# Optimization experiments

Measured on AMD Instinct MI355X. Metric: run time of the kernel, lower is better.

Reference implementation:

```python
import jax, jax.numpy as jnp
import numpy as np
import math

B, S, D, H = 1, 2048, 2048, 16
DH, DHID, DKER = 128, 256, 128  # dim_head, dim_hid, dim_ker


def _uniform(k, shape, a):
    return jax.random.uniform(k, shape, jnp.float32, -a, a)


def setup_inputs() -> dict:
    key = jax.random.key(0)
    ks = jax.random.split(key, 14)
    a1 = math.sqrt(6.0 / (DH + DHID))
    a2 = math.sqrt(6.0 / (DKER + DHID))
    a3 = math.sqrt(6.0 / (2 * DKER))
    return {
        "x_t": jax.random.normal(ks[0], (B, S, D), jnp.float32),
        "q": jax.random.normal(ks[1], (B, S, D), jnp.float32),
        "k": jax.random.normal(ks[2], (B, S, D), jnp.float32),
        "v": jax.random.normal(ks[3], (B, S, D), jnp.float32),
        "lr_attn_mask": jax.random.bernoulli(ks[4], 0.5, (B, H, S, S)),
        "sparse_norms_lse": jax.random.normal(ks[5], (B, H, S, 1), jnp.float32),
        "sparse_attn_weights": jax.random.normal(ks[6], (B, H, S, S), jnp.float32),
        "lambda_constant": 0,
        "kernel_q_mat1": _uniform(ks[7], (H, DH, DHID), a1),
        "kernel_k_mat1": _uniform(ks[8], (H, DH, DHID), a1),
        "kernel_q_mat2": _uniform(ks[9], (H, DHID, DKER), a2),
        "kernel_k_mat2": _uniform(ks[10], (H, DHID, DKER), a2),
        "interaction_k": _uniform(ks[11], (H, DKER, DKER), a3),
        "scalingD": jnp.full((1, H, 1, DKER), 1e-4, jnp.float32),
        "scalingD2": jnp.full((1, H, 1, DKER), 1e-4, jnp.float32),
    }


def _gelu(x):
    return jax.nn.gelu(x, approximate=False)  # matches torch F.gelu default


def reference(x_t, q, k, v, lr_attn_mask, sparse_norms_lse, sparse_attn_weights,
              lambda_constant, kernel_q_mat1, kernel_k_mat1, kernel_q_mat2,
              kernel_k_mat2, interaction_k, scalingD, scalingD2):
    Bq, Sq, Dq = q.shape
    dh = Dq // H
    # [B,S,D] -> [B,H,S,dh]
    qh = q.reshape(Bq, Sq, H, dh).transpose(0, 2, 1, 3)
    kh = k.reshape(Bq, Sq, H, dh).transpose(0, 2, 1, 3)
    vh = v.reshape(Bq, Sq, H, dh).transpose(0, 2, 1, 3)

    # per-head two-layer feature maps (dropout is identity at eval)
    qf = _gelu(jnp.einsum('bhsd,hde->bhse', qh, kernel_q_mat1))
    qf = _gelu(jnp.einsum('bhse,hef->bhsf', qf, kernel_q_mat2))
    kf = _gelu(jnp.einsum('bhsd,hde->bhse', kh, kernel_k_mat1))
    kf = jnp.abs(scalingD) * _gelu(jnp.einsum('bhse,hef->bhsf', kf, kernel_k_mat2))
    kf = kf + jnp.einsum('bhse,hef->bhsf', kf, interaction_k) * scalingD2

    # masked non-negative kernel scores [B,H,S,S]
    scores = jnp.einsum('bhse,bhte->bhst', jnp.abs(qf), jnp.abs(kf))
    m = lr_attn_mask.astype(scores.dtype)
    scores = m * scores

    lr_norms_lse = jnp.log(scores.sum(axis=-1, keepdims=True) + 1e-6)
    norm_factor_lse = jnp.logaddexp(lr_norms_lse, sparse_norms_lse)

    logits = jnp.log(scores + 1e-6) * m + (1.0 - m) * sparse_attn_weights
    attn = jnp.exp(logits - norm_factor_lse)

    out = jnp.einsum('bhst,bhtd->bhsd', attn, vh)
    return out.transpose(0, 2, 1, 3).reshape(Bq, Sq, Dq)
```

## Files before the change

kernel.cpp:

```cpp
#include <hip/hip_runtime.h>
#include <hip/hip_bf16.h>
#include <math.h>

#define H_    16
#define S_    2048
#define D_    2048
#define DH_   128
#define DHID_ 256
#define DKER_ 128

typedef __attribute__((ext_vector_type(8))) short short8v;
typedef __attribute__((ext_vector_type(4))) float float4v;
typedef __attribute__((ext_vector_type(4))) int int4v;

static __device__ __forceinline__ short f2bf(float x){
  union { float f; unsigned u; } v; v.f = x;
  unsigned r = v.u + 0x7fffu + ((v.u >> 16) & 1u);
  return (short)(r >> 16);
}
static __device__ __forceinline__ float gelu_f(float x){
  return 0.5f * x * (1.0f + erff(x * 0.70710678118654752440f));
}
static __device__ __forceinline__ float4v mfma16(short8v a, short8v b, float4v c){
  return __builtin_amdgcn_mfma_f32_16x16x32_bf16(a, b, c, 0, 0, 0);
}
static __device__ __forceinline__ unsigned cvtpk(float lo, float hi){
  unsigned d;
  asm("v_cvt_pk_bf16_f32 %0, %1, %2" : "=v"(d) : "v"(lo), "v"(hi));
  return d;
}
static __device__ __forceinline__ void glds16(const void* g, void* l){
  __builtin_amdgcn_global_load_lds(
      (const __attribute__((address_space(1))) void*)g,
      (__attribute__((address_space(3))) void*)l, 16, 0, 0);
}

__global__ void detect_mask_kernel(const unsigned int* mw, int* flag){
  int t = threadIdx.x;
  int bin = 1, f32ok = 1, odd0 = 1;
  for (int i = t; i < 1024; i += 256){
    unsigned w = mw[i];
    if (w > 1u) bin = 0;
    if (w != 0u && w != 0x3F800000u) f32ok = 0;
    if ((i & 1) && w != 0u) odd0 = 0;
  }
  __shared__ int sb, sf, so;
  if (t == 0){ sb = 1; sf = 1; so = 1; }
  __syncthreads();
  if (!bin)  atomicAnd(&sb, 0);
  if (!f32ok) atomicAnd(&sf, 0);
  if (!odd0) atomicAnd(&so, 0);
  __syncthreads();
  if (t == 0) *flag = sb ? (so ? 3 : 0) : (sf ? 2 : 1);
}

__global__ __launch_bounds__(256) void prep_kernel(
    const void* __restrict__ mask, const int* __restrict__ flagp,
    unsigned* __restrict__ MP,
    const float* __restrict__ w1q, short* __restrict__ W1qT,
    const float* __restrict__ w1k, short* __restrict__ W1kT,
    const float* __restrict__ w2q, short* __restrict__ W2qT,
    const float* __restrict__ w2k, short* __restrict__ W2kT,
    const float* __restrict__ ik,  short* __restrict__ IKT,
    const float* __restrict__ v,   short* __restrict__ V2){
  __shared__ float tile[32][33];
  int b = blockIdx.x;
  int tid = threadIdx.x;

  if (b < 8192){
    int flag = *flagp;
    size_t w = (size_t)b * 256 + tid;
    size_t base = w * 32;
    unsigned bits = 0;
    if (flag == 0){
      const int4v* m = (const int4v*)((const int*)mask + base);
      #pragma unroll
      for (int c = 0; c < 8; ++c){
        int4v x = m[c];
        bits |= (x[0] != 0 ? 1u : 0u) << (c*4+0);
        bits |= (x[1] != 0 ? 1u : 0u) << (c*4+1);
        bits |= (x[2] != 0 ? 1u : 0u) << (c*4+2);
        bits |= (x[3] != 0 ? 1u : 0u) << (c*4+3);
      }
    } else if (flag == 1){
      const int4v* m = (const int4v*)((const unsigned char*)mask + base);
      #pragma unroll
      for (int c = 0; c < 2; ++c){
        int4v x = m[c];
        #pragma unroll
        for (int e = 0; e < 4; ++e){
          unsigned u = (unsigned)x[e];
          #pragma unroll
          for (int bb = 0; bb < 4; ++bb)
            bits |= (((u >> (8*bb)) & 0xffu) != 0 ? 1u : 0u) << (c*16 + e*4 + bb);
        }
      }
    } else if (flag == 2){
      const float4v* m = (const float4v*)((const float*)mask + base);
      #pragma unroll
      for (int c = 0; c < 8; ++c){
        float4v x = m[c];
        bits |= (x[0] != 0.0f ? 1u : 0u) << (c*4+0);
        bits |= (x[1] != 0.0f ? 1u : 0u) << (c*4+1);
        bits |= (x[2] != 0.0f ? 1u : 0u) << (c*4+2);
        bits |= (x[3] != 0.0f ? 1u : 0u) << (c*4+3);
      }
    } else {
      const int4v* m = (const int4v*)((const int*)mask + 2*base);
      #pragma unroll
      for (int c = 0; c < 16; ++c){
        int4v x = m[c];
        bits |= (x[0] != 0 ? 1u : 0u) << (c*2+0);
        bits |= (x[2] != 0 ? 1u : 0u) << (c*2+1);
      }
    }
    MP[w] = bits;
    return;
  }
  b -= 8192;
  if (b < 2048){
    int h = b >> 7, bx = b & 127;
    int d = tid & 127, oct = tid >> 7;
    int t8 = bx * 2 + oct;
    const float* src = v + (size_t)(t8 * 8) * D_ + h * DH_ + d;
    short8v o;
    #pragma unroll
    for (int j = 0; j < 8; ++j) o[j] = f2bf(src[(size_t)j * D_]);
    *(short8v*)(V2 + (((size_t)h * (S_/8) + t8) * DH_ + d) * 8) = o;
    return;
  }
  b -= 2048;
  const float* src; short* dst; int R, C, bx, by, h;
  if (b < 512){        src = w1q; dst = W1qT; R = DH_;  C = DHID_;
                       bx = b & 7; by = (b >> 3) & 3; h = b >> 5; }
  else if (b < 1024){  b -= 512;  src = w1k; dst = W1kT; R = DH_;  C = DHID_;
                       bx = b & 7; by = (b >> 3) & 3; h = b >> 5; }
  else if (b < 1536){  b -= 1024; src = w2q; dst = W2qT; R = DHID_; C = DKER_;
                       bx = b & 3; by = (b >> 2) & 7; h = b >> 5; }
  else if (b < 2048){  b -= 1536; src = w2k; dst = W2kT; R = DHID_; C = DKER_;
                       bx = b & 3; by = (b >> 2) & 7; h = b >> 5; }
  else {               b -= 2048; src = ik;  dst = IKT;  R = DKER_; C = DKER_;
                       bx = b & 3; by = (b >> 2) & 3; h = b >> 4; }
  int tx = tid & 31, ty = tid >> 5;
  int c0 = bx * 32, r0 = by * 32;
  const float* s = src + (size_t)h * R * C;
  short* d = dst + (size_t)h * R * C;
  #pragma unroll
  for (int i = 0; i < 32; i += 8)
    tile[ty + i][tx] = s[(size_t)(r0 + ty + i) * C + (c0 + tx)];
  __syncthreads();
  #pragma unroll
  for (int i = 0; i < 32; i += 8)
    d[(size_t)(c0 + ty + i) * R + (r0 + tx)] = f2bf(tile[tx][ty + i]);
}

__global__ __launch_bounds__(256) void feat_kernel(
    const float* __restrict__ q, const float* __restrict__ k,
    const short* __restrict__ W1qT, const short* __restrict__ W2qT,
    const short* __restrict__ W1kT, const short* __restrict__ W2kT,
    const short* __restrict__ IKT, const float* __restrict__ sD,
    const float* __restrict__ sD2,
    short* __restrict__ QF, short* __restrict__ KF){
  __shared__ __align__(16) short yls[4][16][264];
  int z = blockIdx.y;
  bool isq = z < 16;
  int h = z & 15;
  const float* X = isq ? q : k;
  const short* W1T = isq ? W1qT : W1kT;
  const short* W2T = isq ? W2qT : W2kT;
  int lane = threadIdx.x & 63, warp = threadIdx.x >> 6;
  int s0 = (blockIdx.x * 4 + warp) * 16;
  int col = lane & 15, rg = lane >> 4;
  short8v a[4];
  {
    const float* xr = X + (size_t)(s0 + col) * D_ + h * DH_;
    #pragma unroll
    for (int kb = 0; kb < 4; ++kb){
      int k0 = kb * 32 + rg * 8;
      float4v x0 = *(const float4v*)(xr + k0);
      float4v x1 = *(const float4v*)(xr + k0 + 4);
      short8v t;
      t[0]=f2bf(x0[0]); t[1]=f2bf(x0[1]); t[2]=f2bf(x0[2]); t[3]=f2bf(x0[3]);
      t[4]=f2bf(x1[0]); t[5]=f2bf(x1[1]); t[6]=f2bf(x1[2]); t[7]=f2bf(x1[3]);
      a[kb] = t;
    }
  }
  const short* wbase = W1T + (size_t)h * DHID_ * DH_;
  #pragma unroll
  for (int j = 0; j < 16; ++j){
    int n = j * 16;
    float4v c = {0.f, 0.f, 0.f, 0.f};
    const short* wr = wbase + (size_t)(n + col) * DH_ + rg * 8;
    #pragma unroll
    for (int kb = 0; kb < 4; ++kb)
      c = mfma16(a[kb], *(const short8v*)(wr + kb * 32), c);
    #pragma unroll
    for (int r = 0; r < 4; ++r)
      yls[warp][rg * 4 + r][n + col] = f2bf(gelu_f(c[r]));
  }
  short8v a2[8];
  #pragma unroll
  for (int kb = 0; kb < 8; ++kb)
    a2[kb] = *(const short8v*)(&yls[warp][col][kb * 32 + rg * 8]);
  const short* wb2 = W2T + (size_t)h * DKER_ * DHID_;

  if (isq){
    short* qb = QF + ((size_t)h * S_ + s0) * DKER_;
    #pragma unroll
    for (int j = 0; j < 8; ++j){
      int n = j * 16;
      float4v c = {0.f, 0.f, 0.f, 0.f};
      const short* wr = wb2 + (size_t)(n + col) * DHID_ + rg * 8;
      #pragma unroll
      for (int kb = 0; kb < 8; ++kb)
        c = mfma16(a2[kb], *(const short8v*)(wr + kb * 32), c);
      #pragma unroll
      for (int r = 0; r < 4; ++r)
        qb[(size_t)(rg * 4 + r) * DKER_ + n + col] = f2bf(fabsf(gelu_f(c[r])));
    }
    return;
  }
  float kf0[8][4];
  #pragma unroll
  for (int j = 0; j < 8; ++j){
    int n = j * 16;
    float4v c = {0.f, 0.f, 0.f, 0.f};
    const short* wr = wb2 + (size_t)(n + col) * DHID_ + rg * 8;
    #pragma unroll
    for (int kb = 0; kb < 8; ++kb)
      c = mfma16(a2[kb], *(const short8v*)(wr + kb * 32), c);
    float sc = fabsf(sD[h * DKER_ + n + col]);
    #pragma unroll
    for (int r = 0; r < 4; ++r) kf0[j][r] = sc * gelu_f(c[r]);
  }
  #pragma unroll
  for (int j = 0; j < 8; ++j)
    #pragma unroll
    for (int r = 0; r < 4; ++r)
      yls[warp][rg * 4 + r][j * 16 + col] = f2bf(kf0[j][r]);
  short8v pa[4];
  #pragma unroll
  for (int kb = 0; kb < 4; ++kb)
    pa[kb] = *(const short8v*)(&yls[warp][col][kb * 32 + rg * 8]);
  const short* ib = IKT + (size_t)h * DKER_ * DKER_;
  short* ko = KF + ((size_t)h * S_ + s0) * DKER_;
  #pragma unroll
  for (int j = 0; j < 8; ++j){
    int n = j * 16;
    float4v c = {0.f, 0.f, 0.f, 0.f};
    const short* ir = ib + (size_t)(n + col) * DKER_ + rg * 8;
    #pragma unroll
    for (int kb = 0; kb < 4; ++kb)
      c = mfma16(pa[kb], *(const short8v*)(ir + kb * 32), c);
    float s2 = sD2[h * DKER_ + n + col];
    #pragma unroll
    for (int r = 0; r < 4; ++r)
      ko[(size_t)(rg * 4 + r) * DKER_ + n + col] = f2bf(fabsf(kf0[j][r] + c[r] * s2));
  }
}

__global__ __launch_bounds__(512, 4) void main_attn_kernel(
    const short* __restrict__ QF, const short* __restrict__ KF,
    const short* __restrict__ V2, const unsigned* __restrict__ MP,
    const float* __restrict__ SW, const float* __restrict__ LSE,
    float* __restrict__ OUT){
  __shared__ __align__(16) char smem[65536];
  int tid = threadIdx.x;
  int lane = tid & 63, warp = tid >> 6;
  int hf = warp >> 2, w4 = warp & 3;
  int flat = blockIdx.y * 32 + blockIdx.x;
  int nf = (flat & 7) * 64 + (flat >> 3);
  int sblk = nf & 31, h = nf >> 5;
  int tbase = hf * (S_ / 2);
  int s0 = (sblk * 4 + w4) * 16;
  int col = lane & 15, rg = lane >> 4;

  short* kbuf = (short*)(smem + hf * 32768);
  short* vbuf = (short*)(smem + hf * 32768 + 16384);

  short8v qa[4];
  const short* qr = QF + ((size_t)h * S_ + s0 + col) * DKER_ + rg * 8;
  #pragma unroll
  for (int kb = 0; kb < 4; ++kb) qa[kb] = *(const short8v*)(qr + kb * 32);

  float4v acc[8];
  #pragma unroll
  for (int j = 0; j < 8; ++j) acc[j] = (float4v){0.f, 0.f, 0.f, 0.f};
  float rs = 0.f;

  const char* kf_base = (const char*)(KF + ((size_t)h * S_ + tbase) * DKER_);
  const char* v2_base = (const char*)(V2 + ((size_t)h * (S_/8) + (tbase >> 3)) * DH_ * 8);
  int c0 = w4 * 64 + lane, c1 = c0 + 256;
  int kg0 = (c0 * 16) ^ (((c0 >> 4) & 7) << 4);
  int kg1 = (c1 * 16) ^ (((c1 >> 4) & 7) << 4);
  int vg0 = c0 * 16, vg1 = c1 * 16;
  int lds_lo = w4 * 512, lds_hi = 2048 + w4 * 512;

  const float* swrow = SW + ((size_t)h * S_ + s0 + col) * S_ + tbase + rg * 4;
  const unsigned* mpr = MP + ((size_t)h * S_ + s0 + col) * (S_ / 32) + (tbase >> 5);

  {
    glds16(kf_base + kg0, &kbuf[lds_lo]);
    glds16(kf_base + kg1, &kbuf[lds_hi]);
    glds16(v2_base + vg0, &vbuf[lds_lo]);
    glds16(v2_base + vg1, &vbuf[lds_hi]);
  }
  __syncthreads();

  int swz = (col & 7) << 4;
  int rowb0 = col * 256 + rg * 16;
  int ga = col + ((2 * (rg & 1)) << 4);
  int gb = ga + 16;
  bool hi = (rg >= 2);
  const int NITER = (S_ / 2) / 32;

  for (int ti = 0; ti < NITER; ++ti){
    int cur = ti & 1;
    if (ti + 1 < NITER){
      const char* kt = kf_base + (size_t)(ti + 1) * 8192;
      const char* vt = v2_base + (size_t)(ti + 1) * 8192;
      glds16(kt + kg0, &kbuf[(cur ^ 1) * 4096 + lds_lo]);
      glds16(kt + kg1, &kbuf[(cur ^ 1) * 4096 + lds_hi]);
      glds16(vt + vg0, &vbuf[(cur ^ 1) * 4096 + lds_lo]);
      glds16(vt + vg1, &vbuf[(cur ^ 1) * 4096 + lds_hi]);
    }
    const char* kbp = (const char*)kbuf + cur * 8192;
    const char* vbp = (const char*)vbuf + cur * 8192;

    float4v q0 = {0.f,0.f,0.f,0.f}, q1 = {0.f,0.f,0.f,0.f};
    #pragma unroll
    for (int kk = 0; kk < 4; ++kk){
      short8v a0 = *(const short8v*)(kbp + ((rowb0 + kk * 64) ^ swz));
      short8v a1 = *(const short8v*)(kbp + ((rowb0 + 4096 + kk * 64) ^ swz));
      q0 = mfma16(a0, qa[kk], q0);
      q1 = mfma16(a1, qa[kk], q1);
    }

    const float* swp = swrow + ti * 32;
    float4v sv0 = *(const float4v*)swp;
    float4v sv1 = *(const float4v*)(swp + 16);
    unsigned mw = mpr[ti];
    float p0[4], p1[4];
    #pragma unroll
    for (int r = 0; r < 4; ++r){
      bool m0 = (mw >> (rg * 4 + r)) & 1u;
      bool m1 = (mw >> (16 + rg * 4 + r)) & 1u;
      p0[r] = m0 ? (q0[r] + 1e-6f) : __expf(sv0[r]);
      p1[r] = m1 ? (q1[r] + 1e-6f) : __expf(sv1[r]);
      if (m0) rs += q0[r];
      if (m1) rs += q1[r];
    }
    unsigned k00 = cvtpk(p0[0], p0[1]), k01 = cvtpk(p0[2], p0[3]);
    unsigned k10 = cvtpk(p1[0], p1[1]), k11 = cvtpk(p1[2], p1[3]);
    unsigned a0 = __shfl((int)k00, ga), b0 = __shfl((int)k10, ga);
    unsigned a1 = __shfl((int)k01, ga), b1 = __shfl((int)k11, ga);
    unsigned a2 = __shfl((int)k00, gb), b2 = __shfl((int)k10, gb);
    unsigned a3 = __shfl((int)k01, gb), b3 = __shfl((int)k11, gb);
    union { unsigned u[4]; short8v v8; } pw;
    pw.u[0] = hi ? b0 : a0; pw.u[1] = hi ? b1 : a1;
    pw.u[2] = hi ? b2 : a2; pw.u[3] = hi ? b3 : a3;
    short8v pa = pw.v8;

    #pragma unroll
    for (int j = 0; j < 8; ++j){
      short8v vf = *(const short8v*)(vbp + rg * 2048 + (j * 16 + col) * 16);
      acc[j] = mfma16(pa, vf, acc[j]);
    }
    __syncthreads();
  }

  rs += __shfl_xor(rs, 16);
  rs += __shfl_xor(rs, 32);

  __syncthreads();
  float* cb = (float*)smem;
  float* rb = (float*)(smem + 32768);
  if (hf == 1){
    float* cw = cb + (size_t)w4 * 16 * 128;
    #pragma unroll
    for (int j = 0; j < 8; ++j)
      #pragma unroll
      for (int r = 0; r < 4; ++r)
        cw[(size_t)(rg * 4 + r) * 128 + j * 16 + col] = acc[j][r];
    if (lane < 16) rb[w4 * 16 + lane] = rs;
  }
  __syncthreads();
  if (hf == 0){
    float* cw = cb + (size_t)w4 * 16 * 128;
    #pragma unroll
    for (int j = 0; j < 8; ++j)
      #pragma unroll
      for (int r = 0; r < 4; ++r)
        acc[j][r] += cw[(size_t)(rg * 4 + r) * 128 + j * 16 + col];
    rs += rb[w4 * 16 + col];

    float a = logf(rs + 1e-6f);
    float b = LSE[h * S_ + s0 + col];
    float mx = fmaxf(a, b);
    float sc_col = expf(-(mx + log1pf(expf(-fabsf(a - b)))));
    float scale[4];
    #pragma unroll
    for (int r = 0; r < 4; ++r) scale[r] = __shfl(sc_col, rg * 4 + r);
    float* ob = OUT + (size_t)s0 * D_ + h * DH_;
    #pragma unroll
    for (int j = 0; j < 8; ++j)
      #pragma unroll
      for (int r = 0; r < 4; ++r)
        ob[(size_t)(rg * 4 + r) * D_ + j * 16 + col] = acc[j][r] * scale[r];
  }
}

extern "C" void kernel_launch(void* const* d_in, const int* in_sizes, int n_in,
                              void* d_out, int out_size, void* d_ws, size_t ws_size,
                              hipStream_t stream){
  (void)in_sizes; (void)n_in; (void)out_size; (void)ws_size;
  const float* q   = (const float*)d_in[1];
  const float* k   = (const float*)d_in[2];
  const float* v   = (const float*)d_in[3];
  const void*  msk = d_in[4];
  const float* lse = (const float*)d_in[5];
  const float* sw  = (const float*)d_in[6];
  const float* w1q = (const float*)d_in[8];
  const float* w1k = (const float*)d_in[9];
  const float* w2q = (const float*)d_in[10];
  const float* w2k = (const float*)d_in[11];
  const float* ik  = (const float*)d_in[12];
  const float* sD  = (const float*)d_in[13];
  const float* sD2 = (const float*)d_in[14];
  float* out = (float*)d_out;

  char* ws = (char*)d_ws;
  size_t o = 0;
  int*   flag = (int*)(ws);            o += 256;
  short* W1qT = (short*)(ws + o);      o += (size_t)H_ * DHID_ * DH_ * 2;
  short* W1kT = (short*)(ws + o);      o += (size_t)H_ * DHID_ * DH_ * 2;
  short* W2qT = (short*)(ws + o);      o += (size_t)H_ * DKER_ * DHID_ * 2;
  short* W2kT = (short*)(ws + o);      o += (size_t)H_ * DKER_ * DHID_ * 2;
  short* IKT  = (short*)(ws + o);      o += (size_t)H_ * DKER_ * DKER_ * 2;
  short* V2   = (short*)(ws + o);      o += (size_t)S_ * D_ * 2;
  short* QFb  = (short*)(ws + o);      o += (size_t)H_ * S_ * DKER_ * 2;
  short* KFb  = (short*)(ws + o);      o += (size_t)H_ * S_ * DKER_ * 2;
  unsigned* MP = (unsigned*)(ws + o);  o += (size_t)H_ * S_ * (S_/32) * 4;

  detect_mask_kernel<<<1, 256, 0, stream>>>((const unsigned int*)msk, flag);
  prep_kernel<<<12544, 256, 0, stream>>>(msk, flag, MP,
      w1q, W1qT, w1k, W1kT, w2q, W2qT, w2k, W2kT, ik, IKT, v, V2);

  feat_kernel<<<dim3(S_/64, 32), 256, 0, stream>>>(q, k,
      W1qT, W2qT, W1kT, W2kT, IKT, sD, sD2, QFb, KFb);

  main_attn_kernel<<<dim3(32, 16), 512, 0, stream>>>(
      QFb, KFb, V2, MP, sw, lse, out);
}
```

Baseline: 248.4 us.

## Fold mask detection into prep, prefetch sparse weights, permute V to drop shuffles

Drops the separate single-block mask-format detection kernel; every mask-packing block of prep_kernel now recomputes the format flag from the first 1024 words, saving a launch and the serialized dependency. The V bf16 packing is permuted so each lane's P fragment already matches the MFMA B-operand ordering, which removes the eight cross-lane shuffles and selects per iteration in the attention loop. The sparse-weight and mask-bit loads for the next tile are issued one iteration ahead to hide global latency. This adds redundant detection reads in 8192 blocks and extra registers for the prefetched values.

```diff
diff --git a/kernel.cpp b/kernel.cpp
--- a/kernel.cpp
+++ b/kernel.cpp
@@ -35,27 +35,8 @@
       (__attribute__((address_space(3))) void*)l, 16, 0, 0);
 }
 
-__global__ void detect_mask_kernel(const unsigned int* mw, int* flag){
-  int t = threadIdx.x;
-  int bin = 1, f32ok = 1, odd0 = 1;
-  for (int i = t; i < 1024; i += 256){
-    unsigned w = mw[i];
-    if (w > 1u) bin = 0;
-    if (w != 0u && w != 0x3F800000u) f32ok = 0;
-    if ((i & 1) && w != 0u) odd0 = 0;
-  }
-  __shared__ int sb, sf, so;
-  if (t == 0){ sb = 1; sf = 1; so = 1; }
-  __syncthreads();
-  if (!bin)  atomicAnd(&sb, 0);
-  if (!f32ok) atomicAnd(&sf, 0);
-  if (!odd0) atomicAnd(&so, 0);
-  __syncthreads();
-  if (t == 0) *flag = sb ? (so ? 3 : 0) : (sf ? 2 : 1);
-}
-
 __global__ __launch_bounds__(256) void prep_kernel(
-    const void* __restrict__ mask, const int* __restrict__ flagp,
+    const void* __restrict__ mask,
     unsigned* __restrict__ MP,
     const float* __restrict__ w1q, short* __restrict__ W1qT,
     const float* __restrict__ w1k, short* __restrict__ W1kT,
@@ -64,11 +45,30 @@
     const float* __restrict__ ik,  short* __restrict__ IKT,
     const float* __restrict__ v,   short* __restrict__ V2){
   __shared__ float tile[32][33];
+  __shared__ int sb, sf, so, sflag;
   int b = blockIdx.x;
   int tid = threadIdx.x;
 
   if (b < 8192){
-    int flag = *flagp;
+    {
+      const unsigned* mw = (const unsigned*)mask;
+      int bin = 1, f32ok = 1, odd0 = 1;
+      for (int i = tid; i < 1024; i += 256){
+        unsigned w = mw[i];
+        if (w > 1u) bin = 0;
+        if (w != 0u && w != 0x3F800000u) f32ok = 0;
+        if ((i & 1) && w != 0u) odd0 = 0;
+      }
+      if (tid == 0){ sb = 1; sf = 1; so = 1; }
+      __syncthreads();
+      if (!bin)  atomicAnd(&sb, 0);
+      if (!f32ok) atomicAnd(&sf, 0);
+      if (!odd0) atomicAnd(&so, 0);
+      __syncthreads();
+      if (tid == 0) sflag = sb ? (so ? 3 : 0) : (sf ? 2 : 1);
+      __syncthreads();
+    }
+    int flag = sflag;
     size_t w = (size_t)b * 256 + tid;
     size_t base = w * 32;
     unsigned bits = 0;
@@ -122,11 +122,15 @@
     int h = b >> 7, bx = b & 127;
     int d = tid & 127, oct = tid >> 7;
     int t8 = bx * 2 + oct;
-    const float* src = v + (size_t)(t8 * 8) * D_ + h * DH_ + d;
-    short8v o;
-    #pragma unroll
-    for (int j = 0; j < 8; ++j) o[j] = f2bf(src[(size_t)j * D_]);
-    *(short8v*)(V2 + (((size_t)h * (S_/8) + t8) * DH_ + d) * 8) = o;
+    int t32 = t8 >> 2, o = t8 & 3;
+    const float* src = v + (size_t)(t32 * 32) * D_ + h * DH_ + d;
+    short8v ov;
+    #pragma unroll
+    for (int j = 0; j < 8; ++j){
+      int trel = o * 4 + (j & 3) + ((j >> 2) << 4);
+      ov[j] = f2bf(src[(size_t)trel * D_]);
+    }
+    *(short8v*)(V2 + (((size_t)h * (S_/8) + t8) * DH_ + d) * 8) = ov;
     return;
   }
   b -= 2048;
@@ -305,17 +309,18 @@
     glds16(v2_base + vg0, &vbuf[lds_lo]);
     glds16(v2_base + vg1, &vbuf[lds_hi]);
   }
+  float4v sv0 = *(const float4v*)swrow;
+  float4v sv1 = *(const float4v*)(swrow + 16);
+  unsigned mw = mpr[0];
   __syncthreads();
 
   int swz = (col & 7) << 4;
   int rowb0 = col * 256 + rg * 16;
-  int ga = col + ((2 * (rg & 1)) << 4);
-  int gb = ga + 16;
-  bool hi = (rg >= 2);
   const int NITER = (S_ / 2) / 32;
 
   for (int ti = 0; ti < NITER; ++ti){
     int cur = ti & 1;
+    float4v nsv0, nsv1; unsigned nmw;
     if (ti + 1 < NITER){
       const char* kt = kf_base + (size_t)(ti + 1) * 8192;
       const char* vt = v2_base + (size_t)(ti + 1) * 8192;
@@ -323,6 +328,10 @@
       glds16(kt + kg1, &kbuf[(cur ^ 1) * 4096 + lds_hi]);
       glds16(vt + vg0, &vbuf[(cur ^ 1) * 4096 + lds_lo]);
       glds16(vt + vg1, &vbuf[(cur ^ 1) * 4096 + lds_hi]);
+      const float* swp = swrow + (ti + 1) * 32;
+      nsv0 = *(const float4v*)swp;
+      nsv1 = *(const float4v*)(swp + 16);
+      nmw = mpr[ti + 1];
     }
     const char* kbp = (const char*)kbuf + cur * 8192;
     const char* vbp = (const char*)vbuf + cur * 8192;
@@ -336,10 +345,6 @@
       q1 = mfma16(a1, qa[kk], q1);
     }
 
-    const float* swp = swrow + ti * 32;
-    float4v sv0 = *(const float4v*)swp;
-    float4v sv1 = *(const float4v*)(swp + 16);
-    unsigned mw = mpr[ti];
     float p0[4], p1[4];
     #pragma unroll
     for (int r = 0; r < 4; ++r){
@@ -350,15 +355,9 @@
       if (m0) rs += q0[r];
       if (m1) rs += q1[r];
     }
-    unsigned k00 = cvtpk(p0[0], p0[1]), k01 = cvtpk(p0[2], p0[3]);
-    unsigned k10 = cvtpk(p1[0], p1[1]), k11 = cvtpk(p1[2], p1[3]);
-    unsigned a0 = __shfl((int)k00, ga), b0 = __shfl((int)k10, ga);
-    unsigned a1 = __shfl((int)k01, ga), b1 = __shfl((int)k11, ga);
-    unsigned a2 = __shfl((int)k00, gb), b2 = __shfl((int)k10, gb);
-    unsigned a3 = __shfl((int)k01, gb), b3 = __shfl((int)k11, gb);
     union { unsigned u[4]; short8v v8; } pw;
-    pw.u[0] = hi ? b0 : a0; pw.u[1] = hi ? b1 : a1;
-    pw.u[2] = hi ? b2 : a2; pw.u[3] = hi ? b3 : a3;
+    pw.u[0] = cvtpk(p0[0], p0[1]); pw.u[1] = cvtpk(p0[2], p0[3]);
+    pw.u[2] = cvtpk(p1[0], p1[1]); pw.u[3] = cvtpk(p1[2], p1[3]);
     short8v pa = pw.v8;
 
     #pragma unroll
@@ -367,6 +366,7 @@
       acc[j] = mfma16(pa, vf, acc[j]);
     }
     __syncthreads();
+    sv0 = nsv0; sv1 = nsv1; mw = nmw;
   }
 
   rs += __shfl_xor(rs, 16);
@@ -431,7 +431,7 @@
 
   char* ws = (char*)d_ws;
   size_t o = 0;
-  int*   flag = (int*)(ws);            o += 256;
+  o += 256;
   short* W1qT = (short*)(ws + o);      o += (size_t)H_ * DHID_ * DH_ * 2;
   short* W1kT = (short*)(ws + o);      o += (size_t)H_ * DHID_ * DH_ * 2;
   short* W2qT = (short*)(ws + o);      o += (size_t)H_ * DKER_ * DHID_ * 2;
@@ -442,8 +442,7 @@
   short* KFb  = (short*)(ws + o);      o += (size_t)H_ * S_ * DKER_ * 2;
   unsigned* MP = (unsigned*)(ws + o);  o += (size_t)H_ * S_ * (S_/32) * 4;
 
-  detect_mask_kernel<<<1, 256, 0, stream>>>((const unsigned int*)msk, flag);
-  prep_kernel<<<12544, 256, 0, stream>>>(msk, flag, MP,
+  prep_kernel<<<12544, 256, 0, stream>>>(msk, MP,
       w1q, W1qT, w1k, W1kT, w2q, W2qT, w2k, W2kT, ik, IKT, v, V2);
 
   feat_kernel<<<dim3(S_/64, 32), 256, 0, stream>>>(q, k,
```

Result: slower. 264.8 us (+6.6%).
